# Performance work log

Measured on AMD Instinct MI355X. Metric: run time of the kernel, lower is better.

Reference implementation:

```python
import jax, jax.numpy as jnp
import numpy as np
from functools import partial

B, S, V, E, H = 32, 48, 32000, 512, 512


def setup_inputs() -> dict:
    key = jax.random.key(0)
    ks = jax.random.split(key, 8)
    s = 0.02
    return {
        "encoded": jax.random.normal(ks[0], (B, E), jnp.float32),
        "emb": jax.random.normal(ks[1], (V, E), jnp.float32) * s,   # embedding table
        "Wi": jax.random.normal(ks[2], (4 * H, E), jnp.float32) * s,  # input->gates
        "Wh": jax.random.normal(ks[3], (4 * H, H), jnp.float32) * s,  # hidden->gates
        "bi": jnp.zeros((4 * H,), jnp.float32),
        "bh": jnp.zeros((4 * H,), jnp.float32),
        "Wo": jax.random.normal(ks[4], (V, H), jnp.float32) * s,   # hidden->vocab logits
        "bo": jnp.zeros((V,), jnp.float32),
        "seq_length": S,
    }


def reference(encoded, emb, Wi, Wh, bi, bh, Wo, bo, seq_length):
    """Batched autoregressive decode (teacher_forcing=False path).

    Each step: LSTM cell -> log_softmax over vocab -> store (if still active)
    -> multinomial sample -> embed sampled token as next input. Early EOS
    (token == V-2) is handled by masking stored log-probs to zero thereafter,
    matching the original loop that leaves probs rows as zeros after break.
    """
    bsz = encoded.shape[0]
    hid = Wh.shape[1]
    vocab = Wo.shape[0]
    bias = bi + bh

    def step(carry, k):
        x, h, c, active = carry
        gates = x @ Wi.T + h @ Wh.T + bias          # [B, 4H]
        i_g, f_g, g_g, o_g = jnp.split(gates, 4, axis=-1)  # torch gate order i,f,g,o
        i_g = jax.nn.sigmoid(i_g)
        f_g = jax.nn.sigmoid(f_g)
        g_g = jnp.tanh(g_g)
        o_g = jax.nn.sigmoid(o_g)
        c = f_g * c + i_g * g_g
        h = o_g * jnp.tanh(c)
        logp = jax.nn.log_softmax(h @ Wo.T + bo, axis=-1)  # [B, V]
        stored = jnp.where(active[:, None], logp, 0.0)
        it = jax.random.categorical(k, logp, axis=-1)      # multinomial(exp(logp))
        active = active & (it != vocab - 2)                # EOS token check
        x = emb[it]                                        # next-step input
        return (x, h, c, active), stored

    keys = jax.random.split(jax.random.key(42), seq_length)
    init = (encoded,
            jnp.zeros((bsz, hid), encoded.dtype),
            jnp.zeros((bsz, hid), encoded.dtype),
            jnp.ones((bsz,), bool))
    _, probs = jax.lax.scan(step, init, keys)              # [S, B, V]
    return jnp.transpose(probs, (1, 0, 2))                 # [B, S, V]
```

## Files before the change

kernel.cpp:

```cpp
#include <hip/hip_runtime.h>
#include <stdint.h>
#include <math.h>
#include <limits.h>


#define SEQ 48
#define BSZ 32
#define VOC 32000
#define EDIM 512
#define HDIM 512
#define GDIM 2048
#define KTOT 1024
#define EOS_TOK (VOC - 2)

#define JAX_PARTITIONABLE 1

__device__ __forceinline__ void threefry2x32(uint32_t k0, uint32_t k1,
                                             uint32_t x0, uint32_t x1,
                                             uint32_t& o0, uint32_t& o1)
{
  uint32_t ks2 = k0 ^ k1 ^ 0x1BD11BDAu;
  x0 += k0; x1 += k1;
#define TFR(r) x0 += x1; x1 = (x1 << (r)) | (x1 >> (32 - (r))); x1 ^= x0;
  TFR(13) TFR(15) TFR(26) TFR(6)
  x0 += k1; x1 += ks2 + 1u;
  TFR(17) TFR(29) TFR(16) TFR(24)
  x0 += ks2; x1 += k0 + 2u;
  TFR(13) TFR(15) TFR(26) TFR(6)
  x0 += k0; x1 += k1 + 3u;
  TFR(17) TFR(29) TFR(16) TFR(24)
  x0 += k1; x1 += ks2 + 4u;
  TFR(13) TFR(15) TFR(26) TFR(6)
  x0 += ks2; x1 += k0 + 5u;
#undef TFR
  o0 = x0; o1 = x1;
}

__device__ __forceinline__ uint32_t tf_bits(uint32_t k0, uint32_t k1, uint32_t m)
{
#if JAX_PARTITIONABLE
  uint32_t o0, o1;
  threefry2x32(k0, k1, 0u, m, o0, o1);
  return o0 ^ o1;
#else
  const uint32_t half = (BSZ * VOC) / 2;
  uint32_t o0, o1;
  if (m < half) { threefry2x32(k0, k1, m, m + half, o0, o1); return o0; }
  else          { threefry2x32(k0, k1, m - half, m, o0, o1); return o1; }
#endif
}

__device__ __forceinline__ float gumbel_from_bits(uint32_t bits)
{
  uint32_t fb = (bits >> 9) | 0x3F800000u;
  float u = __uint_as_float(fb) - 1.0f;
  u = fmaxf(u, 1.1754943508222875e-38f);
  return -logf(-logf(u));
}

__device__ __forceinline__ float sigmoidf(float v) { return 1.0f / (1.0f + expf(-v)); }

__global__ __launch_bounds__(256) void init_kernel(
    const float* __restrict__ encoded, float* __restrict__ h0,
    float* __restrict__ c, float* __restrict__ x,
    int* __restrict__ active, uint32_t* __restrict__ keys)
{
  int i = blockIdx.x * 256 + threadIdx.x;
  if (i < BSZ * HDIM) { h0[i] = 0.0f; c[i] = 0.0f; x[i] = encoded[i]; }
  if (blockIdx.x == 0) {
    int t = threadIdx.x;
    if (t < BSZ) active[t] = 1;
    if (t < SEQ) {
#if JAX_PARTITIONABLE
      uint32_t o0, o1;
      threefry2x32(0u, 42u, 0u, (uint32_t)t, o0, o1);
      keys[2 * t] = o0; keys[2 * t + 1] = o1;
#else
      uint32_t a0, a1, b0, b1;
      if (t < 24) {
        threefry2x32(0u, 42u, (uint32_t)(2 * t),     (uint32_t)(2 * t + 48), a0, a1);
        threefry2x32(0u, 42u, (uint32_t)(2 * t + 1), (uint32_t)(2 * t + 49), b0, b1);
        keys[2 * t] = a0; keys[2 * t + 1] = b0;
      } else {
        int i0 = 2 * t - 48, i1 = 2 * t - 47;
        threefry2x32(0u, 42u, (uint32_t)i0, (uint32_t)(i0 + 48), a0, a1);
        threefry2x32(0u, 42u, (uint32_t)i1, (uint32_t)(i1 + 48), b0, b1);
        keys[2 * t] = a1; keys[2 * t + 1] = b1;
      }
#endif
    }
  }
}

__global__ void transpose_kernel(const float* __restrict__ src, float* __restrict__ dst,
                                 int R, int C, int dstLD, int cOff)
{
  __shared__ float tile[32][33];
  int cb = blockIdx.x * 32, rb = blockIdx.y * 32;
  int tx = threadIdx.x, ty = threadIdx.y;
  for (int j = ty; j < 32; j += 8) {
    int r = rb + j, cc = cb + tx;
    if (r < R && cc < C) tile[j][tx] = src[(size_t)r * C + cc];
  }
  __syncthreads();
  for (int j = ty; j < 32; j += 8) {
    int r = rb + tx, cc = cb + j;
    if (r < R && cc < C) dst[(size_t)(cc + cOff) * dstLD + r] = tile[tx][j];
  }
}

__global__ __launch_bounds__(256) void cell_kernel(
    const float* __restrict__ WT,
    const float* __restrict__ bi, const float* __restrict__ bh,
    const float* __restrict__ x, const float* __restrict__ hin,
    float* __restrict__ hout, float* __restrict__ c)
{
  __shared__ float xh[KTOT * 4];
  __shared__ float red[4 * 64 * 4];
  __shared__ float gate[64 * 4];
  int t = threadIdx.x;
  int jc = blockIdx.x;
  int bg = blockIdx.y;
  int bbase = bg * 4;

  for (int i = 0; i < 16; ++i) {
    int idx = i * 256 + t;
    int b = idx >> 10, k = idx & 1023;
    float v = (k < EDIM) ? x[(bbase + b) * EDIM + k]
                         : hin[(bbase + b) * HDIM + (k - EDIM)];
    xh[k * 4 + b] = v;
  }
  __syncthreads();

  int gl = t & 63, kq = t >> 6;
  int type = gl >> 4, jj = gl & 15;
  int gcol = type * 512 + jc * 16 + jj;
  float acc0 = 0.f, acc1 = 0.f, acc2 = 0.f, acc3 = 0.f;
  const float* wp = WT + (size_t)(kq * 256) * GDIM + gcol;
  const float4* xp = (const float4*)xh + kq * 256;
#pragma unroll 8
  for (int k = 0; k < 256; ++k) {
    float w = wp[(size_t)k * GDIM];
    float4 h4 = xp[k];
    acc0 += w * h4.x; acc1 += w * h4.y; acc2 += w * h4.z; acc3 += w * h4.w;
  }
  ((float4*)red)[t] = make_float4(acc0, acc1, acc2, acc3);
  __syncthreads();

  if (t < 64) {
    float4 s0 = ((float4*)red)[t];
    float4 s1 = ((float4*)red)[64 + t];
    float4 s2 = ((float4*)red)[128 + t];
    float4 s3 = ((float4*)red)[192 + t];
    int ty2 = t >> 4, jj2 = t & 15;
    int gc2 = ty2 * 512 + jc * 16 + jj2;
    float bsum = bi[gc2] + bh[gc2];
    float4 g;
    g.x = s0.x + s1.x + s2.x + s3.x + bsum;
    g.y = s0.y + s1.y + s2.y + s3.y + bsum;
    g.z = s0.z + s1.z + s2.z + s3.z + bsum;
    g.w = s0.w + s1.w + s2.w + s3.w + bsum;
    ((float4*)gate)[t] = g;
  }
  __syncthreads();

  if (t < 64) {
    int b = t >> 4, jjf = t & 15;
    float ig = sigmoidf(gate[(0 * 16 + jjf) * 4 + b]);
    float fg = sigmoidf(gate[(1 * 16 + jjf) * 4 + b]);
    float gg = tanhf(  gate[(2 * 16 + jjf) * 4 + b]);
    float og = sigmoidf(gate[(3 * 16 + jjf) * 4 + b]);
    int ci = (bbase + b) * HDIM + jc * 16 + jjf;
    float cn = fg * c[ci] + ig * gg;
    c[ci] = cn;
    hout[ci] = og * tanhf(cn);
  }
}

__global__ __launch_bounds__(256) void logits_kernel(
    const float* __restrict__ WoT,
    const float* __restrict__ bo,
    const float* __restrict__ h,
    const uint32_t* __restrict__ keys, int step,
    float* __restrict__ out,
    float* __restrict__ pmax, float* __restrict__ psum,
    float* __restrict__ pgv, int* __restrict__ pgi)
{
  __shared__ float smem[16384];
  int t = threadIdx.x, bid = blockIdx.x;
  int v0 = bid * 128;
  int vl = t & 63, kq = t >> 6;

  {
    const float4* hp4 = (const float4*)h;
#pragma unroll
    for (int i = 0; i < 16; ++i) {
      int idx4 = i * 256 + t;
      int b = idx4 & 31, k4 = idx4 >> 5;
      float4 v = hp4[b * 128 + k4];
      smem[(k4 * 4 + 0) * 32 + b] = v.x;
      smem[(k4 * 4 + 1) * 32 + b] = v.y;
      smem[(k4 * 4 + 2) * 32 + b] = v.z;
      smem[(k4 * 4 + 3) * 32 + b] = v.w;
    }
  }
  __syncthreads();

  float acc0[32], acc1[32];
#pragma unroll
  for (int b = 0; b < 32; ++b) { acc0[b] = 0.f; acc1[b] = 0.f; }
  const int va = v0 + vl, vb = va + 64;
#pragma unroll 4
  for (int kk = 0; kk < 128; ++kk) {
    int k = kq * 128 + kk;
    float w0 = WoT[(size_t)k * VOC + va];
    float w1 = WoT[(size_t)k * VOC + vb];
    const float4* hp = (const float4*)(smem + k * 32);
#pragma unroll
    for (int bq = 0; bq < 8; ++bq) {
      float4 h4 = hp[bq];
      acc0[bq * 4 + 0] += w0 * h4.x; acc1[bq * 4 + 0] += w1 * h4.x;
      acc0[bq * 4 + 1] += w0 * h4.y; acc1[bq * 4 + 1] += w1 * h4.y;
      acc0[bq * 4 + 2] += w0 * h4.z; acc1[bq * 4 + 2] += w1 * h4.z;
      acc0[bq * 4 + 3] += w0 * h4.w; acc1[bq * 4 + 3] += w1 * h4.w;
    }
  }
  __syncthreads();
#pragma unroll
  for (int b = 0; b < 32; ++b) smem[b * 512 + kq * 128 + vl]      = acc0[b];
#pragma unroll
  for (int b = 0; b < 32; ++b) smem[b * 512 + kq * 128 + 64 + vl] = acc1[b];
  __syncthreads();

  float lg[16];
#pragma unroll
  for (int rep = 0; rep < 16; ++rep) {
    int i = rep * 256 + t;
    int b = i >> 7, vl2 = i & 127;
    float s = smem[b * 512 + 0 * 128 + vl2] + smem[b * 512 + 1 * 128 + vl2]
            + smem[b * 512 + 2 * 128 + vl2] + smem[b * 512 + 3 * 128 + vl2];
    float logit = s + bo[v0 + vl2];
    out[(size_t)b * (SEQ * VOC) + (size_t)step * VOC + v0 + vl2] = logit;
    lg[rep] = logit;
  }
  __syncthreads();
#pragma unroll
  for (int rep = 0; rep < 16; ++rep) {
    int i = rep * 256 + t;
    int b = i >> 7, vl2 = i & 127;
    smem[b * 128 + vl2] = lg[rep];
  }
  __syncthreads();

  int b = t >> 3, l = t & 7;
  float m = -INFINITY;
#pragma unroll
  for (int j = 0; j < 16; ++j) m = fmaxf(m, smem[b * 128 + l + j * 8]);
#pragma unroll
  for (int d = 1; d < 8; d <<= 1) m = fmaxf(m, __shfl_xor(m, d, 64));

  uint32_t k0 = keys[2 * step], k1 = keys[2 * step + 1];
  float ssum = 0.f, gv = -INFINITY;
  int gi = INT_MAX;
#pragma unroll 4
  for (int j = 0; j < 16; ++j) {
    int vl2 = l + j * 8;
    float logit = smem[b * 128 + vl2];
    ssum += expf(logit - m);
    int vg = v0 + vl2;
    uint32_t bits = tf_bits(k0, k1, (uint32_t)(b * VOC + vg));
    float val = logit + gumbel_from_bits(bits);
    if (val > gv || (val == gv && vg < gi)) { gv = val; gi = vg; }
  }
#pragma unroll
  for (int d = 1; d < 8; d <<= 1) {
    ssum += __shfl_xor(ssum, d, 64);
    float ogv = __shfl_xor(gv, d, 64);
    int   ogi = __shfl_xor(gi, d, 64);
    if (ogv > gv || (ogv == gv && ogi < gi)) { gv = ogv; gi = ogi; }
  }
  if (l == 0) {
    pmax[bid * 32 + b] = m;
    psum[bid * 32 + b] = ssum;
    pgv[bid * 32 + b]  = gv;
    pgi[bid * 32 + b]  = gi;
  }
}

__global__ __launch_bounds__(256) void final_kernel(
    const float* __restrict__ pmax, const float* __restrict__ psum,
    const float* __restrict__ pgv, const int* __restrict__ pgi,
    const float* __restrict__ emb, float* __restrict__ x,
    float* __restrict__ lse_s, int* __restrict__ act_s, int* __restrict__ active,
    int step, int nblk)
{
  __shared__ float sm[256], ss[256], sv[256];
  __shared__ int si[256];
  __shared__ int toksh;
  int b = blockIdx.x, t = threadIdx.x;
  float m = -INFINITY, s = 0.f, gv = -INFINITY;
  int gi = INT_MAX;
  if (t < nblk) {
    m = pmax[t * 32 + b]; s = psum[t * 32 + b];
    gv = pgv[t * 32 + b]; gi = pgi[t * 32 + b];
  }
  sm[t] = m; __syncthreads();
  for (int st = 128; st > 0; st >>= 1) {
    if (t < st) sm[t] = fmaxf(sm[t], sm[t + st]);
    __syncthreads();
  }
  float M = sm[0];
  ss[t] = (t < nblk) ? s * expf(m - M) : 0.f;
  sv[t] = gv; si[t] = gi;
  __syncthreads();
  for (int st = 128; st > 0; st >>= 1) {
    if (t < st) {
      ss[t] += ss[t + st];
      if (sv[t + st] > sv[t] || (sv[t + st] == sv[t] && si[t + st] < si[t])) {
        sv[t] = sv[t + st]; si[t] = si[t + st];
      }
    }
    __syncthreads();
  }
  if (t == 0) {
    lse_s[step * 32 + b] = M + logf(ss[0]);
    int tok = si[0];
    act_s[step * 32 + b] = active[b];
    if (tok == EOS_TOK) active[b] = 0;
    toksh = tok;
  }
  __syncthreads();
  int tok = toksh;
  for (int i = t; i < EDIM; i += 256) x[b * EDIM + i] = emb[(size_t)tok * EDIM + i];
}

__global__ __launch_bounds__(256) void finish_kernel(
    float4* __restrict__ out4, const float* __restrict__ lse_s,
    const int* __restrict__ act_s)
{
  const int N4 = BSZ * SEQ * VOC / 4;
  for (int f = blockIdx.x * 256 + threadIdx.x; f < N4; f += gridDim.x * 256) {
    int row = f / (VOC / 4);
    int b = row / SEQ, s = row - b * SEQ;
    int idx = s * 32 + b;
    float4 v = out4[f];
    if (act_s[idx]) {
      float l = lse_s[idx];
      v.x -= l; v.y -= l; v.z -= l; v.w -= l;
    } else {
      v.x = 0.f; v.y = 0.f; v.z = 0.f; v.w = 0.f;
    }
    out4[f] = v;
  }
}

extern "C" void kernel_launch(void* const* d_in, const int* in_sizes, int n_in,
                              void* d_out, int out_size, void* d_ws, size_t ws_size,
                              hipStream_t stream)
{
  (void)in_sizes; (void)n_in; (void)out_size; (void)ws_size;
  const float* encoded = (const float*)d_in[0];
  const float* emb     = (const float*)d_in[1];
  const float* Wi      = (const float*)d_in[2];
  const float* Wh      = (const float*)d_in[3];
  const float* bi      = (const float*)d_in[4];
  const float* bh      = (const float*)d_in[5];
  const float* Wo      = (const float*)d_in[6];
  const float* bo      = (const float*)d_in[7];
  float* out = (float*)d_out;

  float* ws   = (float*)d_ws;
  float* WT   = ws;
  float* WoT  = WT + (size_t)KTOT * GDIM;
  float* h0   = WoT + (size_t)HDIM * VOC;
  float* h1   = h0 + BSZ * HDIM;
  float* c    = h1 + BSZ * HDIM;
  float* x    = c + BSZ * HDIM;
  float* pmax = x + BSZ * EDIM;
  float* psum = pmax + 250 * 32;
  float* pgv  = psum + 250 * 32;
  int*   pgi  = (int*)(pgv + 250 * 32);
  float* lse_s = (float*)(pgi + 250 * 32);
  int*   act_s = (int*)(lse_s + SEQ * BSZ);
  int*   active = act_s + SEQ * BSZ;
  uint32_t* keys = (uint32_t*)(active + BSZ);

  init_kernel<<<dim3(64), dim3(256), 0, stream>>>(encoded, h0, c, x, active, keys);
  transpose_kernel<<<dim3(16, 64),   dim3(32, 8), 0, stream>>>(Wi, WT, GDIM, EDIM, GDIM, 0);
  transpose_kernel<<<dim3(16, 64),   dim3(32, 8), 0, stream>>>(Wh, WT, GDIM, HDIM, GDIM, 512);
  transpose_kernel<<<dim3(16, 1000), dim3(32, 8), 0, stream>>>(Wo, WoT, VOC, HDIM, VOC, 0);

  for (int s = 0; s < SEQ; ++s) {
    float* hin  = (s & 1) ? h1 : h0;
    float* hout = (s & 1) ? h0 : h1;
    cell_kernel<<<dim3(32, 8), dim3(256), 0, stream>>>(WT, bi, bh, x, hin, hout, c);
    logits_kernel<<<dim3(250), dim3(256), 0, stream>>>(WoT, bo, hout, keys, s, out,
                                                       pmax, psum, pgv, pgi);
    final_kernel<<<dim3(32), dim3(256), 0, stream>>>(pmax, psum, pgv, pgi, emb, x,
                                                     lse_s, act_s, active, s, 250);
  }
  finish_kernel<<<dim3(2048), dim3(256), 0, stream>>>((float4*)out, lse_s, act_s);
}
```

Measured before the change: 3.030 ms.

## Use split-bf16 MFMA for vocab logits and fuse final reduction via last-block counter

```diff
diff --git a/kernel.cpp b/kernel.cpp
--- a/kernel.cpp
+++ b/kernel.cpp
@@ -12,8 +12,10 @@
 #define GDIM 2048
 #define KTOT 1024
 #define EOS_TOK (VOC - 2)
-
-#define JAX_PARTITIONABLE 1
+#define NBLK 250
+
+typedef __attribute__((ext_vector_type(8))) short bf16x8;
+typedef __attribute__((ext_vector_type(4))) float f32x4;
 
 __device__ __forceinline__ void threefry2x32(uint32_t k0, uint32_t k1,
                                              uint32_t x0, uint32_t x1,
@@ -38,16 +40,9 @@
 
 __device__ __forceinline__ uint32_t tf_bits(uint32_t k0, uint32_t k1, uint32_t m)
 {
-#if JAX_PARTITIONABLE
   uint32_t o0, o1;
   threefry2x32(k0, k1, 0u, m, o0, o1);
   return o0 ^ o1;
-#else
-  const uint32_t half = (BSZ * VOC) / 2;
-  uint32_t o0, o1;
-  if (m < half) { threefry2x32(k0, k1, m, m + half, o0, o1); return o0; }
-  else          { threefry2x32(k0, k1, m - half, m, o0, o1); return o1; }
-#endif
 }
 
 __device__ __forceinline__ float gumbel_from_bits(uint32_t bits)
@@ -60,10 +55,33 @@
 
 __device__ __forceinline__ float sigmoidf(float v) { return 1.0f / (1.0f + expf(-v)); }
 
+__device__ __forceinline__ unsigned short f2bf(float f) {
+  uint32_t u = __float_as_uint(f);
+  uint32_t r = u + 0x7FFFu + ((u >> 16) & 1u);
+  return (unsigned short)(r >> 16);
+}
+__device__ __forceinline__ float bf2f(unsigned short h) {
+  return __uint_as_float((uint32_t)h << 16);
+}
+
+__device__ __forceinline__ float dlf(const float* p) {
+  return __hip_atomic_load(p, __ATOMIC_RELAXED, __HIP_MEMORY_SCOPE_AGENT);
+}
+__device__ __forceinline__ int dli(const int* p) {
+  return __hip_atomic_load(p, __ATOMIC_RELAXED, __HIP_MEMORY_SCOPE_AGENT);
+}
+__device__ __forceinline__ void dsf(float* p, float v) {
+  __hip_atomic_store(p, v, __ATOMIC_RELAXED, __HIP_MEMORY_SCOPE_AGENT);
+}
+__device__ __forceinline__ void dsi(int* p, int v) {
+  __hip_atomic_store(p, v, __ATOMIC_RELAXED, __HIP_MEMORY_SCOPE_AGENT);
+}
+
 __global__ __launch_bounds__(256) void init_kernel(
     const float* __restrict__ encoded, float* __restrict__ h0,
     float* __restrict__ c, float* __restrict__ x,
-    int* __restrict__ active, uint32_t* __restrict__ keys)
+    int* __restrict__ active, uint32_t* __restrict__ keys,
+    int* __restrict__ counter)
 {
   int i = blockIdx.x * 256 + threadIdx.x;
   if (i < BSZ * HDIM) { h0[i] = 0.0f; c[i] = 0.0f; x[i] = encoded[i]; }
@@ -71,23 +89,10 @@
     int t = threadIdx.x;
     if (t < BSZ) active[t] = 1;
     if (t < SEQ) {
-#if JAX_PARTITIONABLE
+      counter[t] = 0;
       uint32_t o0, o1;
       threefry2x32(0u, 42u, 0u, (uint32_t)t, o0, o1);
       keys[2 * t] = o0; keys[2 * t + 1] = o1;
-#else
-      uint32_t a0, a1, b0, b1;
-      if (t < 24) {
-        threefry2x32(0u, 42u, (uint32_t)(2 * t),     (uint32_t)(2 * t + 48), a0, a1);
-        threefry2x32(0u, 42u, (uint32_t)(2 * t + 1), (uint32_t)(2 * t + 49), b0, b1);
-        keys[2 * t] = a0; keys[2 * t + 1] = b0;
-      } else {
-        int i0 = 2 * t - 48, i1 = 2 * t - 47;
-        threefry2x32(0u, 42u, (uint32_t)i0, (uint32_t)(i0 + 48), a0, a1);
-        threefry2x32(0u, 42u, (uint32_t)i1, (uint32_t)(i1 + 48), b0, b1);
-        keys[2 * t] = a1; keys[2 * t + 1] = b1;
-      }
-#endif
     }
   }
 }
@@ -109,11 +114,33 @@
   }
 }
 
+__global__ __launch_bounds__(256) void wprep_kernel(
+    const float* __restrict__ Wo, unsigned short* __restrict__ WP)
+{
+  int i4 = blockIdx.x * 256 + threadIdx.x;
+  if (i4 >= VOC * 128) return;
+  int v  = i4 >> 7;
+  int k  = (i4 & 127) * 4;
+  const float4 wv = ((const float4*)Wo)[i4];
+  int bid  = v >> 7;
+  int nt   = (v >> 4) & 7;
+  int lane = (v & 15) + (((k >> 3) & 3) << 4);
+  int ks   = k >> 5;
+  int e0   = k & 7;
+  size_t f = (((size_t)bid * 16 + ks) * 8 + nt) * 2;
+  size_t base = f * 512 + (size_t)lane * 8 + e0;
+  unsigned short a0 = f2bf(wv.x), a1 = f2bf(wv.y), a2 = f2bf(wv.z), a3 = f2bf(wv.w);
+  *(ushort4*)(WP + base)       = make_ushort4(a0, a1, a2, a3);
+  *(ushort4*)(WP + base + 512) = make_ushort4(f2bf(wv.x - bf2f(a0)), f2bf(wv.y - bf2f(a1)),
+                                              f2bf(wv.z - bf2f(a2)), f2bf(wv.w - bf2f(a3)));
+}
+
 __global__ __launch_bounds__(256) void cell_kernel(
     const float* __restrict__ WT,
     const float* __restrict__ bi, const float* __restrict__ bh,
     const float* __restrict__ x, const float* __restrict__ hin,
-    float* __restrict__ hout, float* __restrict__ c)
+    float* __restrict__ hout, float* __restrict__ c,
+    unsigned short* __restrict__ h1bf, unsigned short* __restrict__ h2bf)
 {
   __shared__ float xh[KTOT * 4];
   __shared__ float red[4 * 64 * 4];
@@ -173,165 +200,180 @@
     int ci = (bbase + b) * HDIM + jc * 16 + jjf;
     float cn = fg * c[ci] + ig * gg;
     c[ci] = cn;
-    hout[ci] = og * tanhf(cn);
+    float hv = og * tanhf(cn);
+    hout[ci] = hv;
+    unsigned short hh = f2bf(hv);
+    h1bf[ci] = hh;
+    h2bf[ci] = f2bf(hv - bf2f(hh));
   }
 }
 
 __global__ __launch_bounds__(256) void logits_kernel(
-    const float* __restrict__ WoT,
-    const float* __restrict__ bo,
-    const float* __restrict__ h,
+    const bf16x8* __restrict__ WP, const float* __restrict__ bo,
+    const bf16x8* __restrict__ h1v, const bf16x8* __restrict__ h2v,
     const uint32_t* __restrict__ keys, int step,
     float* __restrict__ out,
     float* __restrict__ pmax, float* __restrict__ psum,
-    float* __restrict__ pgv, int* __restrict__ pgi)
-{
-  __shared__ float smem[16384];
-  int t = threadIdx.x, bid = blockIdx.x;
-  int v0 = bid * 128;
-  int vl = t & 63, kq = t >> 6;
-
-  {
-    const float4* hp4 = (const float4*)h;
-#pragma unroll
-    for (int i = 0; i < 16; ++i) {
-      int idx4 = i * 256 + t;
-      int b = idx4 & 31, k4 = idx4 >> 5;
-      float4 v = hp4[b * 128 + k4];
-      smem[(k4 * 4 + 0) * 32 + b] = v.x;
-      smem[(k4 * 4 + 1) * 32 + b] = v.y;
-      smem[(k4 * 4 + 2) * 32 + b] = v.z;
-      smem[(k4 * 4 + 3) * 32 + b] = v.w;
-    }
-  }
-  __syncthreads();
-
-  float acc0[32], acc1[32];
-#pragma unroll
-  for (int b = 0; b < 32; ++b) { acc0[b] = 0.f; acc1[b] = 0.f; }
-  const int va = v0 + vl, vb = va + 64;
-#pragma unroll 4
-  for (int kk = 0; kk < 128; ++kk) {
-    int k = kq * 128 + kk;
-    float w0 = WoT[(size_t)k * VOC + va];
-    float w1 = WoT[(size_t)k * VOC + vb];
-    const float4* hp = (const float4*)(smem + k * 32);
-#pragma unroll
-    for (int bq = 0; bq < 8; ++bq) {
-      float4 h4 = hp[bq];
-      acc0[bq * 4 + 0] += w0 * h4.x; acc1[bq * 4 + 0] += w1 * h4.x;
-      acc0[bq * 4 + 1] += w0 * h4.y; acc1[bq * 4 + 1] += w1 * h4.y;
-      acc0[bq * 4 + 2] += w0 * h4.z; acc1[bq * 4 + 2] += w1 * h4.z;
-      acc0[bq * 4 + 3] += w0 * h4.w; acc1[bq * 4 + 3] += w1 * h4.w;
-    }
-  }
-  __syncthreads();
-#pragma unroll
-  for (int b = 0; b < 32; ++b) smem[b * 512 + kq * 128 + vl]      = acc0[b];
-#pragma unroll
-  for (int b = 0; b < 32; ++b) smem[b * 512 + kq * 128 + 64 + vl] = acc1[b];
-  __syncthreads();
-
-  float lg[16];
-#pragma unroll
-  for (int rep = 0; rep < 16; ++rep) {
-    int i = rep * 256 + t;
-    int b = i >> 7, vl2 = i & 127;
-    float s = smem[b * 512 + 0 * 128 + vl2] + smem[b * 512 + 1 * 128 + vl2]
-            + smem[b * 512 + 2 * 128 + vl2] + smem[b * 512 + 3 * 128 + vl2];
-    float logit = s + bo[v0 + vl2];
-    out[(size_t)b * (SEQ * VOC) + (size_t)step * VOC + v0 + vl2] = logit;
-    lg[rep] = logit;
-  }
-  __syncthreads();
-#pragma unroll
-  for (int rep = 0; rep < 16; ++rep) {
-    int i = rep * 256 + t;
-    int b = i >> 7, vl2 = i & 127;
-    smem[b * 128 + vl2] = lg[rep];
-  }
-  __syncthreads();
-
-  int b = t >> 3, l = t & 7;
-  float m = -INFINITY;
-#pragma unroll
-  for (int j = 0; j < 16; ++j) m = fmaxf(m, smem[b * 128 + l + j * 8]);
-#pragma unroll
-  for (int d = 1; d < 8; d <<= 1) m = fmaxf(m, __shfl_xor(m, d, 64));
-
-  uint32_t k0 = keys[2 * step], k1 = keys[2 * step + 1];
-  float ssum = 0.f, gv = -INFINITY;
-  int gi = INT_MAX;
-#pragma unroll 4
-  for (int j = 0; j < 16; ++j) {
-    int vl2 = l + j * 8;
-    float logit = smem[b * 128 + vl2];
-    ssum += expf(logit - m);
-    int vg = v0 + vl2;
-    uint32_t bits = tf_bits(k0, k1, (uint32_t)(b * VOC + vg));
-    float val = logit + gumbel_from_bits(bits);
-    if (val > gv || (val == gv && vg < gi)) { gv = val; gi = vg; }
-  }
-#pragma unroll
-  for (int d = 1; d < 8; d <<= 1) {
-    ssum += __shfl_xor(ssum, d, 64);
-    float ogv = __shfl_xor(gv, d, 64);
-    int   ogi = __shfl_xor(gi, d, 64);
-    if (ogv > gv || (ogv == gv && ogi < gi)) { gv = ogv; gi = ogi; }
-  }
-  if (l == 0) {
-    pmax[bid * 32 + b] = m;
-    psum[bid * 32 + b] = ssum;
-    pgv[bid * 32 + b]  = gv;
-    pgi[bid * 32 + b]  = gi;
-  }
-}
-
-__global__ __launch_bounds__(256) void final_kernel(
-    const float* __restrict__ pmax, const float* __restrict__ psum,
-    const float* __restrict__ pgv, const int* __restrict__ pgi,
+    float* __restrict__ pgv, int* __restrict__ pgi,
+    int* __restrict__ counter,
     const float* __restrict__ emb, float* __restrict__ x,
-    float* __restrict__ lse_s, int* __restrict__ act_s, int* __restrict__ active,
-    int step, int nblk)
-{
-  __shared__ float sm[256], ss[256], sv[256];
-  __shared__ int si[256];
-  __shared__ int toksh;
-  int b = blockIdx.x, t = threadIdx.x;
-  float m = -INFINITY, s = 0.f, gv = -INFINITY;
-  int gi = INT_MAX;
-  if (t < nblk) {
-    m = pmax[t * 32 + b]; s = psum[t * 32 + b];
-    gv = pgv[t * 32 + b]; gi = pgi[t * 32 + b];
-  }
-  sm[t] = m; __syncthreads();
-  for (int st = 128; st > 0; st >>= 1) {
-    if (t < st) sm[t] = fmaxf(sm[t], sm[t + st]);
+    int* __restrict__ active, float* __restrict__ lse_s, int* __restrict__ act_s)
+{
+  __shared__ float cm[4][32], cs[4][32], cv[4][32];
+  __shared__ int   cidx[4][32];
+  __shared__ float fmx[8][32], fsx[8][32], fvx[8][32];
+  __shared__ int   fix[8][32];
+  __shared__ int   toks[32];
+  __shared__ int   doneflag;
+
+  const int t = threadIdx.x, bid = blockIdx.x;
+  const int w = t >> 6, l = t & 63;
+  const int lr = l & 15, lq = l >> 4;
+  const int v0 = bid * 128;
+
+  f32x4 a00 = {0.f, 0.f, 0.f, 0.f};
+  f32x4 a01 = a00, a10 = a00, a11 = a00;
+
+  const int ab0 = lr * 64 + lq;
+  const int ab1 = (16 + lr) * 64 + lq;
+  const int wb0 = bid * 16384 + (w * 2) * 128 + l;
+
+#pragma unroll 2
+  for (int ks = 0; ks < 16; ++ks) {
+    bf16x8 x10 = h1v[ab0 + ks * 4];
+    bf16x8 x11 = h1v[ab1 + ks * 4];
+    bf16x8 x20 = h2v[ab0 + ks * 4];
+    bf16x8 x21 = h2v[ab1 + ks * 4];
+    const int wb = wb0 + ks * 1024;
+    bf16x8 w10 = WP[wb];
+    bf16x8 w20 = WP[wb + 64];
+    bf16x8 w11 = WP[wb + 128];
+    bf16x8 w21 = WP[wb + 192];
+    a00 = __builtin_amdgcn_mfma_f32_16x16x32_bf16(x10, w10, a00, 0, 0, 0);
+    a01 = __builtin_amdgcn_mfma_f32_16x16x32_bf16(x10, w11, a01, 0, 0, 0);
+    a10 = __builtin_amdgcn_mfma_f32_16x16x32_bf16(x11, w10, a10, 0, 0, 0);
+    a11 = __builtin_amdgcn_mfma_f32_16x16x32_bf16(x11, w11, a11, 0, 0, 0);
+    a00 = __builtin_amdgcn_mfma_f32_16x16x32_bf16(x10, w20, a00, 0, 0, 0);
+    a01 = __builtin_amdgcn_mfma_f32_16x16x32_bf16(x10, w21, a01, 0, 0, 0);
+    a10 = __builtin_amdgcn_mfma_f32_16x16x32_bf16(x11, w20, a10, 0, 0, 0);
+    a11 = __builtin_amdgcn_mfma_f32_16x16x32_bf16(x11, w21, a11, 0, 0, 0);
+    a00 = __builtin_amdgcn_mfma_f32_16x16x32_bf16(x20, w10, a00, 0, 0, 0);
+    a01 = __builtin_amdgcn_mfma_f32_16x16x32_bf16(x20, w11, a01, 0, 0, 0);
+    a10 = __builtin_amdgcn_mfma_f32_16x16x32_bf16(x21, w10, a10, 0, 0, 0);
+    a11 = __builtin_amdgcn_mfma_f32_16x16x32_bf16(x21, w11, a11, 0, 0, 0);
+  }
+
+  const int va = v0 + w * 32 + lr;
+  const int vb = va + 16;
+  const float boa = bo[va], bob = bo[vb];
+  const uint32_t k0 = keys[2 * step], k1 = keys[2 * step + 1];
+
+#pragma unroll
+  for (int mt = 0; mt < 2; ++mt) {
+    const f32x4 A0 = mt ? a10 : a00;
+    const f32x4 A1 = mt ? a11 : a01;
+#pragma unroll
+    for (int reg = 0; reg < 4; ++reg) {
+      const int b = mt * 16 + lq * 4 + reg;
+      const float La = A0[reg] + boa;
+      const float Lb = A1[reg] + bob;
+      size_t obase = (size_t)b * (SEQ * VOC) + (size_t)step * VOC;
+      out[obase + va] = La;
+      out[obase + vb] = Lb;
+
+      float mx = fmaxf(La, Lb);
+      mx = fmaxf(mx, __shfl_xor(mx, 1, 64));
+      mx = fmaxf(mx, __shfl_xor(mx, 2, 64));
+      mx = fmaxf(mx, __shfl_xor(mx, 4, 64));
+      mx = fmaxf(mx, __shfl_xor(mx, 8, 64));
+      float se = expf(La - mx) + expf(Lb - mx);
+
+      uint32_t ba = tf_bits(k0, k1, (uint32_t)(b * VOC + va));
+      uint32_t bb = tf_bits(k0, k1, (uint32_t)(b * VOC + vb));
+      float ga = La + gumbel_from_bits(ba);
+      float gb = Lb + gumbel_from_bits(bb);
+      float gvx; int gix;
+      if (ga >= gb) { gvx = ga; gix = va; } else { gvx = gb; gix = vb; }
+#pragma unroll
+      for (int d = 1; d < 16; d <<= 1) {
+        se += __shfl_xor(se, d, 64);
+        float og = __shfl_xor(gvx, d, 64);
+        int   oi = __shfl_xor(gix, d, 64);
+        if (og > gvx || (og == gvx && oi < gix)) { gvx = og; gix = oi; }
+      }
+      if (lr == 0) {
+        cm[w][b] = mx; cs[w][b] = se; cv[w][b] = gvx; cidx[w][b] = gix;
+      }
+    }
+  }
+  __syncthreads();
+
+  if (t < 32) {
+    const int b = t;
+    float M = cm[0][b];
+    M = fmaxf(M, cm[1][b]); M = fmaxf(M, cm[2][b]); M = fmaxf(M, cm[3][b]);
+    float S = 0.f;
+    float GV = -INFINITY; int GI = INT_MAX;
+#pragma unroll
+    for (int ww = 0; ww < 4; ++ww) {
+      S += cs[ww][b] * expf(cm[ww][b] - M);
+      if (cv[ww][b] > GV || (cv[ww][b] == GV && cidx[ww][b] < GI)) {
+        GV = cv[ww][b]; GI = cidx[ww][b];
+      }
+    }
+    dsf(pmax + bid * 32 + b, M);
+    dsf(psum + bid * 32 + b, S);
+    dsf(pgv  + bid * 32 + b, GV);
+    dsi(pgi  + bid * 32 + b, GI);
+    __threadfence();
+  }
+  __syncthreads();
+  if (t == 0) {
+    int old = __hip_atomic_fetch_add(counter + step, 1, __ATOMIC_ACQ_REL,
+                                     __HIP_MEMORY_SCOPE_AGENT);
+    doneflag = (old == NBLK - 1);
+  }
+  __syncthreads();
+
+  if (doneflag) {
+    __threadfence();
+    const int b = t & 31, j = t >> 5;
+    float M = -INFINITY, S = 0.f, GV = -INFINITY; int GI = INT_MAX;
+    for (int i = j; i < NBLK; i += 8) {
+      float m = dlf(pmax + i * 32 + b);
+      float s = dlf(psum + i * 32 + b);
+      float g = dlf(pgv  + i * 32 + b);
+      int  gi = dli(pgi  + i * 32 + b);
+      float mn = fmaxf(M, m);
+      S = S * expf(M - mn) + s * expf(m - mn);
+      M = mn;
+      if (g > GV || (g == GV && gi < GI)) { GV = g; GI = gi; }
+    }
+    fmx[j][b] = M; fsx[j][b] = S; fvx[j][b] = GV; fix[j][b] = GI;
     __syncthreads();
-  }
-  float M = sm[0];
-  ss[t] = (t < nblk) ? s * expf(m - M) : 0.f;
-  sv[t] = gv; si[t] = gi;
-  __syncthreads();
-  for (int st = 128; st > 0; st >>= 1) {
-    if (t < st) {
-      ss[t] += ss[t + st];
-      if (sv[t + st] > sv[t] || (sv[t + st] == sv[t] && si[t + st] < si[t])) {
-        sv[t] = sv[t + st]; si[t] = si[t + st];
+    if (t < 32) {
+      float M2 = fmx[0][t];
+#pragma unroll
+      for (int jj = 1; jj < 8; ++jj) M2 = fmaxf(M2, fmx[jj][t]);
+      float S2 = 0.f; float GV2 = -INFINITY; int GI2 = INT_MAX;
+#pragma unroll
+      for (int jj = 0; jj < 8; ++jj) {
+        S2 += fsx[jj][t] * expf(fmx[jj][t] - M2);
+        if (fvx[jj][t] > GV2 || (fvx[jj][t] == GV2 && fix[jj][t] < GI2)) {
+          GV2 = fvx[jj][t]; GI2 = fix[jj][t];
+        }
       }
+      lse_s[step * 32 + t] = M2 + logf(S2);
+      act_s[step * 32 + t] = active[t];
+      if (GI2 == EOS_TOK) active[t] = 0;
+      toks[t] = GI2;
     }
     __syncthreads();
-  }
-  if (t == 0) {
-    lse_s[step * 32 + b] = M + logf(ss[0]);
-    int tok = si[0];
-    act_s[step * 32 + b] = active[b];
-    if (tok == EOS_TOK) active[b] = 0;
-    toksh = tok;
-  }
-  __syncthreads();
-  int tok = toksh;
-  for (int i = t; i < EDIM; i += 256) x[b * EDIM + i] = emb[(size_t)tok * EDIM + i];
+    for (int i = t; i < BSZ * 128; i += 256) {
+      int row = i >> 7;
+      ((float4*)x)[i] = ((const float4*)emb)[(size_t)toks[row] * 128 + (i & 127)];
+    }
+  }
 }
 
 __global__ __launch_bounds__(256) void finish_kernel(
@@ -345,8 +387,8 @@
     int idx = s * 32 + b;
     float4 v = out4[f];
     if (act_s[idx]) {
-      float l = lse_s[idx];
-      v.x -= l; v.y -= l; v.z -= l; v.w -= l;
+      float lsv = lse_s[idx];
+      v.x -= lsv; v.y -= lsv; v.z -= lsv; v.w -= lsv;
     } else {
       v.x = 0.f; v.y = 0.f; v.z = 0.f; v.w = 0.f;
     }
@@ -369,35 +411,39 @@
   const float* bo      = (const float*)d_in[7];
   float* out = (float*)d_out;
 
-  float* ws   = (float*)d_ws;
-  float* WT   = ws;
-  float* WoT  = WT + (size_t)KTOT * GDIM;
-  float* h0   = WoT + (size_t)HDIM * VOC;
-  float* h1   = h0 + BSZ * HDIM;
-  float* c    = h1 + BSZ * HDIM;
-  float* x    = c + BSZ * HDIM;
-  float* pmax = x + BSZ * EDIM;
-  float* psum = pmax + 250 * 32;
-  float* pgv  = psum + 250 * 32;
-  int*   pgi  = (int*)(pgv + 250 * 32);
-  float* lse_s = (float*)(pgi + 250 * 32);
-  int*   act_s = (int*)(lse_s + SEQ * BSZ);
-  int*   active = act_s + SEQ * BSZ;
-  uint32_t* keys = (uint32_t*)(active + BSZ);
-
-  init_kernel<<<dim3(64), dim3(256), 0, stream>>>(encoded, h0, c, x, active, keys);
-  transpose_kernel<<<dim3(16, 64),   dim3(32, 8), 0, stream>>>(Wi, WT, GDIM, EDIM, GDIM, 0);
-  transpose_kernel<<<dim3(16, 64),   dim3(32, 8), 0, stream>>>(Wh, WT, GDIM, HDIM, GDIM, 512);
-  transpose_kernel<<<dim3(16, 1000), dim3(32, 8), 0, stream>>>(Wo, WoT, VOC, HDIM, VOC, 0);
+  char* W = (char*)d_ws;
+  size_t off = 0;
+  float* WT = (float*)(W + off);            off += (size_t)KTOT * GDIM * 4;
+  unsigned short* WP = (unsigned short*)(W + off); off += (size_t)VOC * 512 * 2 * 2;
+  float* h0 = (float*)(W + off);            off += BSZ * HDIM * 4;
+  float* h1 = (float*)(W + off);            off += BSZ * HDIM * 4;
+  float* c  = (float*)(W + off);            off += BSZ * HDIM * 4;
+  float* x  = (float*)(W + off);            off += BSZ * EDIM * 4;
+  unsigned short* h1bf = (unsigned short*)(W + off); off += BSZ * HDIM * 2;
+  unsigned short* h2bf = (unsigned short*)(W + off); off += BSZ * HDIM * 2;
+  float* pmax = (float*)(W + off);          off += NBLK * 32 * 4;
+  float* psum = (float*)(W + off);          off += NBLK * 32 * 4;
+  float* pgv  = (float*)(W + off);          off += NBLK * 32 * 4;
+  int*   pgi  = (int*)(W + off);            off += NBLK * 32 * 4;
+  float* lse_s = (float*)(W + off);         off += SEQ * BSZ * 4;
+  int*   act_s = (int*)(W + off);           off += SEQ * BSZ * 4;
+  int*   active = (int*)(W + off);          off += 128;
+  uint32_t* keys = (uint32_t*)(W + off);    off += SEQ * 2 * 4;
+  int*   counter = (int*)(W + off);         off += SEQ * 4;
+
+  init_kernel<<<dim3(64), dim3(256), 0, stream>>>(encoded, h0, c, x, active, keys, counter);
+  transpose_kernel<<<dim3(16, 64), dim3(32, 8), 0, stream>>>(Wi, WT, GDIM, EDIM, GDIM, 0);
+  transpose_kernel<<<dim3(16, 64), dim3(32, 8), 0, stream>>>(Wh, WT, GDIM, HDIM, GDIM, 512);
+  wprep_kernel<<<dim3((VOC * 128 + 255) / 256), dim3(256), 0, stream>>>(Wo, WP);
 
   for (int s = 0; s < SEQ; ++s) {
     float* hin  = (s & 1) ? h1 : h0;
     float* hout = (s & 1) ? h0 : h1;
-    cell_kernel<<<dim3(32, 8), dim3(256), 0, stream>>>(WT, bi, bh, x, hin, hout, c);
-    logits_kernel<<<dim3(250), dim3(256), 0, stream>>>(WoT, bo, hout, keys, s, out,
-                                                       pmax, psum, pgv, pgi);
-    final_kernel<<<dim3(32), dim3(256), 0, stream>>>(pmax, psum, pgv, pgi, emb, x,
-                                                     lse_s, act_s, active, s, 250);
+    cell_kernel<<<dim3(32, 8), dim3(256), 0, stream>>>(WT, bi, bh, x, hin, hout, c,
+                                                       h1bf, h2bf);
+    logits_kernel<<<dim3(NBLK), dim3(256), 0, stream>>>(
+        (const bf16x8*)WP, bo, (const bf16x8*)h1bf, (const bf16x8*)h2bf,
+        keys, s, out, pmax, psum, pgv, pgi, counter, emb, x, active, lse_s, act_s);
   }
   finish_kernel<<<dim3(2048), dim3(256), 0, stream>>>((float4*)out, lse_s, act_s);
 }
```

New measurement: 3.750 ms. 23.8% more time.
